# Performance work log

Hardware: AMD Instinct MI355X
Metric: run time of the kernel (lower is better)

The kernel has to match this reference:

```python
import jax, jax.numpy as jnp
import numpy as np

# Production-scale dims: MD system with 100 atoms, all-pairs distance descriptors,
# single full-dataset batch of 512 frames (module docstring: single batch, no shuffle).
B = 512            # batch (frames)
A = 100            # n_atoms
P = A * (A - 1) // 2   # n_descriptors = 4950 pairwise distances
NNZ = B * P * 6    # each descriptor touches 2 atoms x 3 dims -> 6 nonzeros per (batch, desc)


def setup_inputs() -> dict:
    key = jax.random.key(0)
    k1, k2 = jax.random.split(key)
    # Structured sparsity pattern: descriptor d = distance(pi[d], pj[d]).
    pi, pj = np.triu_indices(A, 1)                         # [P] each
    atom_pat = np.repeat(np.stack([pi, pj], axis=1).reshape(-1), 3)  # [6P]
    dim_pat = np.tile(np.arange(3), 2 * P)                 # [6P]
    des_pat = np.repeat(np.arange(P), 6)                   # [6P]
    batch_ind = np.repeat(np.arange(B), 6 * P)             # [NNZ]
    des_ind = np.tile(des_pat, B)                          # [NNZ]
    flat_pat = atom_pat * 3 + dim_pat                      # atom*3 + dim, [6P]
    # scatter index == batch*(n_atoms*3) + atom*3 + dim (what _get_scatter_indices computes
    # when every (atom, dim) slot is covered)
    scatter_idx = batch_ind * (A * 3) + np.tile(flat_pat, B)
    x = jax.random.normal(k1, (B, P), dtype=jnp.float32)       # dq/d(descriptors)
    left = jax.random.normal(k2, (NNZ,), dtype=jnp.float32)    # nonzero d(desc)/d(pos)
    return {
        "x": x,
        "left": left,
        "batch_ind": jnp.asarray(batch_ind, dtype=jnp.int32),
        "des_ind": jnp.asarray(des_ind, dtype=jnp.int32),
        "scatter_idx": jnp.asarray(scatter_idx, dtype=jnp.int32),
    }


def reference(x, left, batch_ind, des_ind, scatter_idx):
    # gather: right = x[batch_ind, des_ind]   (SmartDerivatives._create_right)
    right = x[batch_ind, des_ind]              # [NNZ]
    src = left * right                         # [NNZ]
    # scatter_sum over flat (batch, atom, dim) slots, then square (chain-rule combine)
    out = jax.ops.segment_sum(src, scatter_idx, num_segments=B * A * 3)
    return jnp.square(out).reshape(B, A * 3)
```

## Files before the change

### kernel.cpp

```cpp
#include <hip/hip_runtime.h>
#include <hip/hip_fp16.h>

#define NB   512
#define NP   4950
#define NG   2475
#define NOUT 300
#define LDC  128
#define BT   1024

__device__ __forceinline__ int rowOf(int p) {
    int i = (int)((199.0f - sqrtf((float)(39601 - 8 * p))) * 0.5f);
    while ((i + 1) * (199 - (i + 1)) / 2 <= p) ++i;
    while (i * (199 - i) / 2 > p) --i;
    return i;
}

__device__ __forceinline__ int a16(int r, int c) {
    return r * LDC + (c ^ (((r >> 1) & 31) << 1));
}

struct GrpL {
    float4 l0, l1, l2;
    float2 xv;
};

__device__ __forceinline__ GrpL loadGrp(const float* __restrict__ lb,
                                        const float2* __restrict__ xb2, int g) {
    GrpL G;
    const float4* lp = (const float4*)(lb + 12 * g);
    G.l0 = lp[0];
    G.l1 = lp[1];
    G.l2 = lp[2];
    G.xv = xb2[g];
    return G;
}

__device__ __forceinline__ void writeGrp(__half* __restrict__ T0,
                                         __half* __restrict__ T1,
                                         __half* __restrict__ T2,
                                         const GrpL& G, int g) {
    const int p0 = 2 * g;
    const int i0 = rowOf(p0);
    const int j0 = p0 - i0 * (199 - i0) / 2 + i0 + 1;
    int i1, j1;
    if (j0 < 99) { i1 = i0;     j1 = j0 + 1; }
    else         { i1 = i0 + 1; j1 = i1 + 1; }

    T0[a16(i0, j0)] = __float2half(G.l0.x * G.xv.x);
    T1[a16(i0, j0)] = __float2half(G.l0.y * G.xv.x);
    T2[a16(i0, j0)] = __float2half(G.l0.z * G.xv.x);
    T0[a16(j0, i0)] = __float2half(G.l0.w * G.xv.x);
    T1[a16(j0, i0)] = __float2half(G.l1.x * G.xv.x);
    T2[a16(j0, i0)] = __float2half(G.l1.y * G.xv.x);

    T0[a16(i1, j1)] = __float2half(G.l1.z * G.xv.y);
    T1[a16(i1, j1)] = __float2half(G.l1.w * G.xv.y);
    T2[a16(i1, j1)] = __float2half(G.l2.x * G.xv.y);
    T0[a16(j1, i1)] = __float2half(G.l2.y * G.xv.y);
    T1[a16(j1, i1)] = __float2half(G.l2.z * G.xv.y);
    T2[a16(j1, i1)] = __float2half(G.l2.w * G.xv.y);
}

__global__ __launch_bounds__(BT, 8)
void smartderiv_hoist(const float* __restrict__ x,
                      const float* __restrict__ left,
                      float* __restrict__ out)
{
    __shared__ __half T3[3][100 * LDC];

    const int b   = blockIdx.x;
    const int tid = threadIdx.x;

    if (tid < 300) {
        const int d = tid / 100, r = tid - 100 * d;
        T3[d][a16(r, r)] = __float2half(0.0f);
    }

    const float*  lb  = left + (size_t)b * (6 * NP);
    const float2* xb2 = (const float2*)(x + (size_t)b * NP);

    const int w = tid >> 6, l = tid & 63;
    const int base = (NG * w) >> 4;
    const int nw   = ((NG * (w + 1)) >> 4) - base;
    const int g0 = base + l;
    const int g1 = base + 64 + l;
    const int g2 = base + 128 + l;
    const bool has2 = (128 + l) < nw;

    GrpL A = loadGrp(lb, xb2, g0);
    GrpL B = loadGrp(lb, xb2, g1);
    GrpL C;
    if (has2) C = loadGrp(lb, xb2, g2);

    __half* T0 = T3[0];
    __half* T1 = T3[1];
    __half* T2 = T3[2];
    writeGrp(T0, T1, T2, A, g0);
    writeGrp(T0, T1, T2, B, g1);
    if (has2) writeGrp(T0, T1, T2, C, g2);

    __syncthreads();

    if (tid < 600) {
        const int q = tid >> 1;
        const int u = tid & 1;
        const int d = q / 100;
        const int r = q - 100 * d;
        const int s = (r >> 1) & 31;
        const __half2* row = (const __half2*)(&T3[d][r * LDC]);

        float acc = 0.0f;
        #pragma unroll
        for (int t = 0; t < 25; ++t) {
            const float2 v = __half22float2(row[(2 * t + u) ^ s]);
            acc += v.x + v.y;
        }
        acc += __shfl_xor(acc, 1);
        if (u == 0) {
            out[(size_t)b * NOUT + r * 3 + d] = acc * acc;
        }
    }
}

extern "C" void kernel_launch(void* const* d_in, const int* in_sizes, int n_in,
                              void* d_out, int out_size, void* d_ws, size_t ws_size,
                              hipStream_t stream) {
    const float* x    = (const float*)d_in[0];
    const float* left = (const float*)d_in[1];
    float* out = (float*)d_out;

    smartderiv_hoist<<<NB, BT, 0, stream>>>(x, left, out);
}
```

Before: 17.86 us.

## Process two batches per block with double-buffered LDS to overlap loads and reduction

Each block now handles two frames using two LDS buffers. The second frame's global loads are issued before the first frame's row reduction and store, so memory latency overlaps LDS work. Group assignment changes from per-wave contiguous ranges to a tid-strided layout, and the grid is halved. In exchange it doubles LDS use per block (about 153KB), which allows at most one block per CU and cuts the number of blocks available to fill the GPU.

After: 17.91 us. About the same (+0.3%).

```diff
diff --git a/kernel.cpp b/kernel.cpp
--- a/kernel.cpp
+++ b/kernel.cpp
@@ -35,16 +35,17 @@
     return G;
 }
 
-__device__ __forceinline__ void writeGrp(__half* __restrict__ T0,
-                                         __half* __restrict__ T1,
-                                         __half* __restrict__ T2,
-                                         const GrpL& G, int g) {
+__device__ __forceinline__ void writeGrp(__half* __restrict__ Tb, const GrpL& G, int g) {
     const int p0 = 2 * g;
     const int i0 = rowOf(p0);
     const int j0 = p0 - i0 * (199 - i0) / 2 + i0 + 1;
     int i1, j1;
     if (j0 < 99) { i1 = i0;     j1 = j0 + 1; }
     else         { i1 = i0 + 1; j1 = i1 + 1; }
+
+    __half* T0 = Tb;
+    __half* T1 = Tb + 100 * LDC;
+    __half* T2 = Tb + 200 * LDC;
 
     T0[a16(i0, j0)] = __float2half(G.l0.x * G.xv.x);
     T1[a16(i0, j0)] = __float2half(G.l0.y * G.xv.x);
@@ -61,53 +62,16 @@
     T2[a16(j1, i1)] = __float2half(G.l2.w * G.xv.y);
 }
 
-__global__ __launch_bounds__(BT, 8)
-void smartderiv_hoist(const float* __restrict__ x,
-                      const float* __restrict__ left,
-                      float* __restrict__ out)
-{
-    __shared__ __half T3[3][100 * LDC];
-
-    const int b   = blockIdx.x;
-    const int tid = threadIdx.x;
-
-    if (tid < 300) {
-        const int d = tid / 100, r = tid - 100 * d;
-        T3[d][a16(r, r)] = __float2half(0.0f);
-    }
-
-    const float*  lb  = left + (size_t)b * (6 * NP);
-    const float2* xb2 = (const float2*)(x + (size_t)b * NP);
-
-    const int w = tid >> 6, l = tid & 63;
-    const int base = (NG * w) >> 4;
-    const int nw   = ((NG * (w + 1)) >> 4) - base;
-    const int g0 = base + l;
-    const int g1 = base + 64 + l;
-    const int g2 = base + 128 + l;
-    const bool has2 = (128 + l) < nw;
-
-    GrpL A = loadGrp(lb, xb2, g0);
-    GrpL B = loadGrp(lb, xb2, g1);
-    GrpL C;
-    if (has2) C = loadGrp(lb, xb2, g2);
-
-    __half* T0 = T3[0];
-    __half* T1 = T3[1];
-    __half* T2 = T3[2];
-    writeGrp(T0, T1, T2, A, g0);
-    writeGrp(T0, T1, T2, B, g1);
-    if (has2) writeGrp(T0, T1, T2, C, g2);
-
-    __syncthreads();
-
+__device__ __forceinline__ void readStore(const __half* __restrict__ Tb,
+                                          float* __restrict__ out,
+                                          int b, int tid) {
     if (tid < 600) {
         const int q = tid >> 1;
         const int u = tid & 1;
         const int d = q / 100;
         const int r = q - 100 * d;
         const int s = (r >> 1) & 31;
-        const __half2* row = (const __half2*)(&T3[d][r * LDC]);
+        const __half2* row = (const __half2*)(Tb + d * (100 * LDC) + r * LDC);
 
         float acc = 0.0f;
         #pragma unroll
@@ -122,6 +86,61 @@
     }
 }
 
+__global__ __launch_bounds__(BT, 4)
+void smartderiv_pipe(const float* __restrict__ x,
+                     const float* __restrict__ left,
+                     float* __restrict__ out)
+{
+    __shared__ __half T[2][3 * 100 * LDC];
+
+    const int blk = blockIdx.x;
+    const int tid = threadIdx.x;
+    const int b0 = 2 * blk;
+    const int b1 = b0 + 1;
+
+    if (tid < 600) {
+        const int buf = (tid >= 300);
+        const int q = tid - 300 * buf;
+        const int d = q / 100, r = q - 100 * d;
+        T[buf][d * (100 * LDC) + a16(r, r)] = __float2half(0.0f);
+    }
+
+    const float*  lb0 = left + (size_t)b0 * (6 * NP);
+    const float2* xb0 = (const float2*)(x + (size_t)b0 * NP);
+    const float*  lb1 = left + (size_t)b1 * (6 * NP);
+    const float2* xb1 = (const float2*)(x + (size_t)b1 * NP);
+
+    const int g0 = tid, g1 = tid + BT, g2 = tid + 2 * BT;
+    const bool has2 = (g2 < NG);
+
+    {
+        GrpL A = loadGrp(lb0, xb0, g0);
+        GrpL B = loadGrp(lb0, xb0, g1);
+        GrpL C;
+        if (has2) C = loadGrp(lb0, xb0, g2);
+        writeGrp(T[0], A, g0);
+        writeGrp(T[0], B, g1);
+        if (has2) writeGrp(T[0], C, g2);
+    }
+
+    __syncthreads();
+
+    GrpL A = loadGrp(lb1, xb1, g0);
+    GrpL B = loadGrp(lb1, xb1, g1);
+    GrpL C;
+    if (has2) C = loadGrp(lb1, xb1, g2);
+
+    readStore(T[0], out, b0, tid);
+
+    writeGrp(T[1], A, g0);
+    writeGrp(T[1], B, g1);
+    if (has2) writeGrp(T[1], C, g2);
+
+    __syncthreads();
+
+    readStore(T[1], out, b1, tid);
+}
+
 extern "C" void kernel_launch(void* const* d_in, const int* in_sizes, int n_in,
                               void* d_out, int out_size, void* d_ws, size_t ws_size,
                               hipStream_t stream) {
@@ -129,5 +148,5 @@
     const float* left = (const float*)d_in[1];
     float* out = (float*)d_out;
 
-    smartderiv_hoist<<<NB, BT, 0, stream>>>(x, left, out);
+    smartderiv_pipe<<<NB / 2, BT, 0, stream>>>(x, left, out);
 }
```
